# Performance work log

Hardware: AMD Instinct MI355X
Metric: run time of the kernel (lower is better)

The kernel has to match this reference:

```python
import jax, jax.numpy as jnp
import numpy as np

KERNEL_SIZE = 2
DILATION = 2


def aconv(x, A, shift):
    # x: [n, c, v, l], A: [v, w]; temporal roll + zero-mask first `shift` steps,
    # then node diffusion x . A over the node axis.
    xr = jnp.roll(x, shift, axis=3)
    if shift > 0:
        xr = xr.at[..., :shift].set(0.0)
    return jnp.einsum('ncvl,vw->ncwl', xr, A)


def setup_inputs() -> dict:
    key = jax.random.key(0)
    ks = jax.random.split(key, 7)
    N, C, V, L, E, CO = 32, 64, 500, 64, 10, 64
    return {
        'x': jax.random.normal(ks[0], (N, C, V, L), dtype=jnp.float32),
        'nodevec1': jax.random.normal(ks[1], (V, E), dtype=jnp.float32),
        'nodevec2': jax.random.normal(ks[2], (E, V), dtype=jnp.float32),
        'et_w': jax.random.normal(ks[3], (E, E), dtype=jnp.float32),
        'et_b': jax.random.normal(ks[4], (E,), dtype=jnp.float32),
        'mlp_w': jax.random.normal(ks[5], (CO, (1 + KERNEL_SIZE) * C), dtype=jnp.float32) * 0.05,
        'mlp_b': jax.random.normal(ks[6], (CO,), dtype=jnp.float32),
    }


def reference(x, nodevec1, nodevec2, et_w, et_b, mlp_w, mlp_b):
    out = [x]
    x2 = x
    shift = 0
    # hop 0: adaptive adjacency from node embeddings
    adp = jax.nn.softmax(jax.nn.relu(nodevec1 @ nodevec2), axis=1)
    x1 = aconv(x2, adp, shift)
    out.append(x1)
    shift = DILATION
    x2 = x1
    for i in range(KERNEL_SIZE - 1):
        # emb_trans: affine update of both node embeddings
        nodevec1 = nodevec1 @ et_w + et_b
        nodevec2 = (nodevec2.T @ et_w + et_b).T
        adp = jax.nn.softmax(jax.nn.relu(nodevec1 @ nodevec2), axis=1)
        x1 = aconv(x2, adp, shift)
        out.append(x1)
        shift = shift + DILATION
        x2 = x1
    h = jnp.concatenate(out, axis=1)  # [n, (1+K)*c, v, l]
    # 1x1 conv == channel matmul; dropout is identity at inference
    h = jnp.einsum('ncvl,oc->novl', h, mlp_w) + mlp_b[None, :, None, None]
    return h
```

## Files before the change

kernel.cpp:

```cpp
#include <hip/hip_runtime.h>
#include <hip/hip_bf16.h>

#define NB 32
#define CC 64
#define VV 500
#define LL 64
#define EE 10
#define CO 64
#define DIL 2
#define VP 512
#define SL (VV * LL)

typedef unsigned short u16;
typedef unsigned int   u32;
typedef __attribute__((ext_vector_type(8))) short bf16x8;
typedef __attribute__((ext_vector_type(4))) float f32x4;

typedef const __attribute__((address_space(1))) void g_void;
typedef __attribute__((address_space(3))) void l_void;

__device__ __forceinline__ float bf2f(u16 u) {
    union { u32 i; float f; } c; c.i = ((u32)u) << 16; return c.f;
}
__device__ __forceinline__ u16 f2bf(float f) {
    union { float f; u32 i; } c; c.f = f;
    u32 x = c.i;
    u32 r = (x + 0x7fffu + ((x >> 16) & 1u)) >> 16;
    return (u16)r;
}

__global__ void emb_kernel(const float* __restrict__ nv1, const float* __restrict__ nv2,
                           const float* __restrict__ et_w, const float* __restrict__ et_b,
                           const float* __restrict__ mlp_w,
                           float* __restrict__ nv1t, float* __restrict__ nv2t,
                           u16* __restrict__ wb) {
    int idx = blockIdx.x * blockDim.x + threadIdx.x;
    if (idx < VV * EE) {
        int v = idx / EE, e = idx - v * EE;
        float s = et_b[e];
        #pragma unroll
        for (int f = 0; f < EE; f++) s += nv1[v * EE + f] * et_w[f * EE + e];
        nv1t[idx] = s;
    } else if (idx < 2 * VV * EE) {
        int k = idx - VV * EE;
        int e = k / VV, v = k - e * VV;
        float s = et_b[e];
        #pragma unroll
        for (int f = 0; f < EE; f++) s += nv2[f * VV + v] * et_w[f * EE + e];
        nv2t[k] = s;
    } else if (idx < 2 * VV * EE + CO * 3 * CC) {
        int k = idx - 2 * VV * EE;
        wb[k] = f2bf(mlp_w[k]);
    }
}

__global__ __launch_bounds__(64) void adj_kernel(const float* __restrict__ p1,
                                                 const float* __restrict__ p2,
                                                 u16* __restrict__ Atb) {
    const int v = blockIdx.x;
    const int lane = threadIdx.x;
    if (v >= VV) {
        #pragma unroll
        for (int j = 0; j < 8; j++) Atb[(size_t)(lane + 64 * j) * VP + v] = 0;
        return;
    }
    float e1[EE];
    #pragma unroll
    for (int e = 0; e < EE; e++) e1[e] = p1[v * EE + e];

    float r[8];
    float m = -1e30f;
    #pragma unroll
    for (int j = 0; j < 8; j++) {
        int w = lane + 64 * j;
        if (w < VV) {
            float s = 0.f;
            #pragma unroll
            for (int e = 0; e < EE; e++) s += e1[e] * p2[e * VV + w];
            r[j] = fmaxf(s, 0.f);
            m = fmaxf(m, r[j]);
        } else {
            r[j] = -1e30f;
        }
    }
    #pragma unroll
    for (int off = 32; off > 0; off >>= 1) m = fmaxf(m, __shfl_xor(m, off));

    float p[8];
    float sum = 0.f;
    #pragma unroll
    for (int j = 0; j < 8; j++) {
        int w = lane + 64 * j;
        if (w < VV) { p[j] = expf(r[j] - m); sum += p[j]; }
    }
    #pragma unroll
    for (int off = 32; off > 0; off >>= 1) sum += __shfl_xor(sum, off);
    float inv = 1.f / sum;
    #pragma unroll
    for (int j = 0; j < 8; j++) {
        int w = lane + 64 * j;
        Atb[(size_t)w * VP + v] = (w < VV) ? f2bf(p[j] * inv) : (u16)0;
    }
}

__global__ __launch_bounds__(512, 2) void hops_fused(const float* __restrict__ x,
                                                     const u16* __restrict__ Atb0,
                                                     const u16* __restrict__ Atb1,
                                                     u16* __restrict__ x1g,
                                                     u16* __restrict__ x2g) {
    __shared__ u16 Xt[LL * VP];
    __shared__ u16 Ab[2][512 * 32];
    const int nc = blockIdx.x;
    const int tid = threadIdx.x;
    const size_t base = (size_t)nc * (VV * LL);
    const int lane = tid & 63;
    const int wv = tid >> 6;

    int ldsoff[4], rowoff[4];
    #pragma unroll
    for (int j = 0; j < 4; ++j) {
        const int lin = j * 8192 + tid * 16;
        const int w = lin >> 6;
        const int cell = ((lin >> 4) & 3) ^ ((w >> 1) & 3);
        ldsoff[j] = lin;
        rowoff[j] = w * VP + cell * 8;
    }
    char* ab0 = (char*)&Ab[0][0];
    char* ab1 = (char*)&Ab[1][0];

    auto issue_chunk = [&](const u16* Asrc, int kb, char* dst) {
        #pragma unroll
        for (int j = 0; j < 4; ++j)
            __builtin_amdgcn_global_load_lds(
                (g_void*)(Asrc + rowoff[j] + kb),
                (l_void*)(dst + ldsoff[j]), 16, 0, 0);
    };

    issue_chunk(Atb0, 0, ab0);

    {
        char* ldsb = (char*)Xt;
        const int lquad = lane & 15;
        const int vsub = lane >> 4;
        const int l0 = 4 * lquad;
        #pragma unroll
        for (int i = 0; i < 8; ++i) {
            const int vp = wv * 32 + i * 4 + vsub;
            const int v0 = 2 * vp;
            u32 pk0, pk1, pk2, pk3;
            if (v0 < VV) {
                const float* xa = x + base + v0 * LL + l0;
                float4 fa = *(const float4*)xa;
                float4 fb = *(const float4*)(xa + LL);
                pk0 = (u32)f2bf(fa.x) | ((u32)f2bf(fb.x) << 16);
                pk1 = (u32)f2bf(fa.y) | ((u32)f2bf(fb.y) << 16);
                pk2 = (u32)f2bf(fa.z) | ((u32)f2bf(fb.z) << 16);
                pk3 = (u32)f2bf(fa.w) | ((u32)f2bf(fb.w) << 16);
            } else {
                pk0 = pk1 = pk2 = pk3 = 0;
            }
            const int vb = 4 * vp;
            int l = l0;
            *(u32*)(ldsb + l * (VP * 2) + (vb ^ ((l & 7) << 4))) = pk0; l++;
            *(u32*)(ldsb + l * (VP * 2) + (vb ^ ((l & 7) << 4))) = pk1; l++;
            *(u32*)(ldsb + l * (VP * 2) + (vb ^ ((l & 7) << 4))) = pk2; l++;
            *(u32*)(ldsb + l * (VP * 2) + (vb ^ ((l & 7) << 4))) = pk3;
        }
    }
    __syncthreads();

    const int wr = wv * 64;
    const int r15 = lane & 15;
    const int kg = lane >> 4;
    const char* ldsb = (const char*)Xt;
    int lrow[4], lswz[4], aoff[4];
    #pragma unroll
    for (int ct = 0; ct < 4; ct++) {
        const int l = ct * 16 + r15;
        lrow[ct] = l * (VP * 2);
        lswz[ct] = (l & 7) << 4;
    }
    #pragma unroll
    for (int rt = 0; rt < 4; rt++) {
        const int w = wr + rt * 16 + r15;
        aoff[rt] = w * 64 + ((kg ^ ((w >> 1) & 3)) << 4);
    }

    f32x4 acc[4][4];
    #pragma unroll
    for (int rt = 0; rt < 4; rt++)
        #pragma unroll
        for (int ct = 0; ct < 4; ct++)
            acc[rt][ct] = (f32x4){0.f, 0.f, 0.f, 0.f};

    #pragma unroll
    for (int s = 0; s < 16; ++s) {
        const int g1 = s + 1;
        issue_chunk(g1 < 16 ? Atb0 : Atb1, (g1 & 15) * 32, (g1 & 1) ? ab1 : ab0);

        const char* ac = (s & 1) ? ab1 : ab0;
        bf16x8 a[4], b[4];
        #pragma unroll
        for (int rt = 0; rt < 4; rt++)
            a[rt] = *(const bf16x8*)(ac + aoff[rt]);
        #pragma unroll
        for (int ct = 0; ct < 4; ct++)
            b[ct] = *(const bf16x8*)(ldsb + lrow[ct] + ((s * 64 + kg * 16) ^ lswz[ct]));
        #pragma unroll
        for (int rt = 0; rt < 4; rt++)
            #pragma unroll
            for (int ct = 0; ct < 4; ct++)
                acc[rt][ct] = __builtin_amdgcn_mfma_f32_16x16x32_bf16(a[rt], b[ct], acc[rt][ct], 0, 0, 0);
        __syncthreads();
    }

    {
        u16* xo = x1g + base;
        #pragma unroll
        for (int rt = 0; rt < 4; rt++) {
            #pragma unroll
            for (int ct = 0; ct < 4; ct++) {
                const int col = ct * 16 + r15;
                const int wbase = wr + rt * 16 + kg * 4;
                f32x4 c = acc[rt][ct];
                #pragma unroll
                for (int r = 0; r < 4; r++) {
                    int w = wbase + r;
                    if (w < VV) xo[w * LL + col] = f2bf(c[r]);
                }
            }
        }
    }

    {
        char* ldsw = (char*)Xt;
        {
            const int l = tid >> 8;
            const int j = tid & 255;
            *(u32*)(ldsw + l * (VP * 2) + 4 * j) = 0;
        }
        #pragma unroll
        for (int rt = 0; rt < 4; rt++) {
            const int wb2 = (wr + rt * 16 + kg * 4) * 2;
            #pragma unroll
            for (int ct = 0; ct < 4; ct++) {
                const int col = ct * 16 + r15;
                const int ln = col + DIL;
                if (ln < LL) {
                    f32x4 c = acc[rt][ct];
                    u32 plo = (u32)f2bf(c[0]) | ((u32)f2bf(c[1]) << 16);
                    u32 phi = (u32)f2bf(c[2]) | ((u32)f2bf(c[3]) << 16);
                    const int swz = (ln & 7) << 4;
                    char* p = ldsw + ln * (VP * 2);
                    *(u32*)(p + (wb2 ^ swz)) = plo;
                    *(u32*)(p + ((wb2 + 4) ^ swz)) = phi;
                }
            }
        }
    }
    __syncthreads();

    #pragma unroll
    for (int rt = 0; rt < 4; rt++)
        #pragma unroll
        for (int ct = 0; ct < 4; ct++)
            acc[rt][ct] = (f32x4){0.f, 0.f, 0.f, 0.f};

    #pragma unroll
    for (int s = 0; s < 16; ++s) {
        const int g = 16 + s;
        const int g1 = g + 1;
        if (g1 < 32)
            issue_chunk(Atb1, (g1 & 15) * 32, (g1 & 1) ? ab1 : ab0);

        const char* ac = (g & 1) ? ab1 : ab0;
        bf16x8 a[4], b[4];
        #pragma unroll
        for (int rt = 0; rt < 4; rt++)
            a[rt] = *(const bf16x8*)(ac + aoff[rt]);
        #pragma unroll
        for (int ct = 0; ct < 4; ct++)
            b[ct] = *(const bf16x8*)(ldsb + lrow[ct] + ((s * 64 + kg * 16) ^ lswz[ct]));
        #pragma unroll
        for (int rt = 0; rt < 4; rt++)
            #pragma unroll
            for (int ct = 0; ct < 4; ct++)
                acc[rt][ct] = __builtin_amdgcn_mfma_f32_16x16x32_bf16(a[rt], b[ct], acc[rt][ct], 0, 0, 0);
        __syncthreads();
    }

    {
        u16* xo = x2g + base;
        #pragma unroll
        for (int rt = 0; rt < 4; rt++) {
            #pragma unroll
            for (int ct = 0; ct < 4; ct++) {
                const int col = ct * 16 + r15;
                const int wbase = wr + rt * 16 + kg * 4;
                f32x4 c = acc[rt][ct];
                #pragma unroll
                for (int r = 0; r < 4; r++) {
                    int w = wbase + r;
                    if (w < VV) xo[w * LL + col] = f2bf(c[r]);
                }
            }
        }
    }
}

__global__ __launch_bounds__(256, 3) void mlp_mfma(const float* __restrict__ x,
                                                   const u16* __restrict__ x1,
                                                   const u16* __restrict__ x2,
                                                   const u16* __restrict__ wb,
                                                   const float* __restrict__ b,
                                                   float* __restrict__ out) {
    __shared__ u16 Ht[128 * 192];
    const int bid = blockIdx.x;
    const int n = bid / (SL / 128);
    const int st = bid - n * (SL / 128);
    const int s0 = st * 128;
    const int tid = threadIdx.x;

    const int lane = tid & 63;
    const int wv = tid >> 6;
    const int obase = (wv & 1) * 32;
    const int sbase = (wv >> 1) * 64;
    const int r15 = lane & 15;
    const int kg = lane >> 4;

    bf16x8 afrag[2][6];
    #pragma unroll
    for (int rt = 0; rt < 2; rt++)
        #pragma unroll
        for (int ks = 0; ks < 6; ks++)
            afrag[rt][ks] = *(const bf16x8*)(wb + (obase + rt * 16 + r15) * (3 * CC) + ks * 32 + kg * 8);

    {
        char* ldsb = (char*)Ht;
        const int squad = tid >> 3;
        const int pgroup = tid & 7;
        const int sq0 = 4 * squad;
        #pragma unroll
        for (int i = 0; i < 12; ++i) {
            const int P = i * 8 + pgroup;
            const int c = 2 * P;
            u32 pk0, pk1, pk2, pk3;
            if (i < 4) {
                const float* fsrc = x + ((size_t)n * CC + c) * SL + s0 + sq0;
                float4 va = *(const float4*)fsrc;
                float4 vb = *(const float4*)(fsrc + SL);
                pk0 = (u32)f2bf(va.x) | ((u32)f2bf(vb.x) << 16);
                pk1 = (u32)f2bf(va.y) | ((u32)f2bf(vb.y) << 16);
                pk2 = (u32)f2bf(va.z) | ((u32)f2bf(vb.z) << 16);
                pk3 = (u32)f2bf(va.w) | ((u32)f2bf(vb.w) << 16);
            } else {
                const u16* bsrc = (i < 8)
                    ? x1 + ((size_t)n * CC + (c - CC)) * SL + s0 + sq0
                    : x2 + ((size_t)n * CC + (c - 2 * CC)) * SL + s0 + sq0;
                uint2 va = *(const uint2*)bsrc;
                uint2 vb = *(const uint2*)(bsrc + SL);
                pk0 = (va.x & 0xffffu) | (vb.x << 16);
                pk1 = (va.x >> 16) | (vb.x & 0xffff0000u);
                pk2 = (va.y & 0xffffu) | (vb.y << 16);
                pk3 = (va.y >> 16) | (vb.y & 0xffff0000u);
            }
            int s = sq0;
            *(u32*)(ldsb + s * 384 + ((4 * P) ^ ((s & 7) << 4))) = pk0; s++;
            *(u32*)(ldsb + s * 384 + ((4 * P) ^ ((s & 7) << 4))) = pk1; s++;
            *(u32*)(ldsb + s * 384 + ((4 * P) ^ ((s & 7) << 4))) = pk2; s++;
            *(u32*)(ldsb + s * 384 + ((4 * P) ^ ((s & 7) << 4))) = pk3;
        }
    }
    __syncthreads();

    f32x4 acc[2][4];
    #pragma unroll
    for (int rt = 0; rt < 2; rt++)
        #pragma unroll
        for (int ct = 0; ct < 4; ct++)
            acc[rt][ct] = (f32x4){0.f, 0.f, 0.f, 0.f};

    const char* ldsb = (const char*)Ht;
    #pragma unroll
    for (int ks = 0; ks < 6; ks++) {
        bf16x8 bfr[4];
        #pragma unroll
        for (int ct = 0; ct < 4; ct++) {
            const int s = sbase + ct * 16 + r15;
            bfr[ct] = *(const bf16x8*)(ldsb + s * 384 + ((ks * 64 + kg * 16) ^ ((s & 7) << 4)));
        }
        #pragma unroll
        for (int rt = 0; rt < 2; rt++)
            #pragma unroll
            for (int ct = 0; ct < 4; ct++)
                acc[rt][ct] = __builtin_amdgcn_mfma_f32_16x16x32_bf16(afrag[rt][ks], bfr[ct], acc[rt][ct], 0, 0, 0);
    }

    #pragma unroll
    for (int rt = 0; rt < 2; rt++) {
        #pragma unroll
        for (int r = 0; r < 4; r++) {
            const int o = obase + rt * 16 + kg * 4 + r;
            const float bias = b[o];
            float* orow = out + ((size_t)n * CO + o) * SL + s0 + sbase;
            #pragma unroll
            for (int ct = 0; ct < 4; ct++)
                orow[ct * 16 + r15] = acc[rt][ct][r] + bias;
        }
    }
}

extern "C" void kernel_launch(void* const* d_in, const int* in_sizes, int n_in,
                              void* d_out, int out_size, void* d_ws, size_t ws_size,
                              hipStream_t stream) {
    const float* x     = (const float*)d_in[0];
    const float* nv1   = (const float*)d_in[1];
    const float* nv2   = (const float*)d_in[2];
    const float* et_w  = (const float*)d_in[3];
    const float* et_b  = (const float*)d_in[4];
    const float* mlp_w = (const float*)d_in[5];
    const float* mlp_b = (const float*)d_in[6];
    float* out = (float*)d_out;

    char* wsb = (char*)d_ws;
    size_t off = 0;
    auto alloc = [&](size_t bytes) {
        size_t o = off;
        off += (bytes + 255) & ~(size_t)255;
        return o;
    };
    u16*   Atb0 = (u16*)(wsb + alloc((size_t)VP * VP * 2));
    u16*   Atb1 = (u16*)(wsb + alloc((size_t)VP * VP * 2));
    float* nv1t = (float*)(wsb + alloc((size_t)VV * EE * 4));
    float* nv2t = (float*)(wsb + alloc((size_t)EE * VV * 4));
    u16*   wb   = (u16*)(wsb + alloc((size_t)CO * 3 * CC * 2));
    u16*   x1   = (u16*)(wsb + alloc((size_t)NB * CC * VV * LL * 2));
    u16*   x2   = (u16*)(wsb + alloc((size_t)NB * CC * VV * LL * 2));
    (void)in_sizes; (void)n_in; (void)out_size; (void)ws_size;

    const int embN = 2 * VV * EE + CO * 3 * CC;
    emb_kernel<<<(embN + 255) / 256, 256, 0, stream>>>(nv1, nv2, et_w, et_b, mlp_w, nv1t, nv2t, wb);
    adj_kernel<<<VP, 64, 0, stream>>>(nv1, nv2, Atb0);
    adj_kernel<<<VP, 64, 0, stream>>>(nv1t, nv2t, Atb1);
    hops_fused<<<NB * CC, 512, 0, stream>>>(x, Atb0, Atb1, x1, x2);
    mlp_mfma<<<NB * (SL / 128), 256, 0, stream>>>(x, x1, x2, wb, mlp_b, out);
}
```

Baseline: 510.7 us.

## Triple-buffer adjacency chunks with prefetch distance two and explicit waitcnt barriers

```diff
diff --git a/kernel.cpp b/kernel.cpp
--- a/kernel.cpp
+++ b/kernel.cpp
@@ -109,7 +109,7 @@
                                                      u16* __restrict__ x1g,
                                                      u16* __restrict__ x2g) {
     __shared__ u16 Xt[LL * VP];
-    __shared__ u16 Ab[2][512 * 32];
+    __shared__ u16 Ab[3][512 * 32];
     const int nc = blockIdx.x;
     const int tid = threadIdx.x;
     const size_t base = (size_t)nc * (VV * LL);
@@ -125,8 +125,7 @@
         ldsoff[j] = lin;
         rowoff[j] = w * VP + cell * 8;
     }
-    char* ab0 = (char*)&Ab[0][0];
-    char* ab1 = (char*)&Ab[1][0];
+    char* abuf[3] = { (char*)&Ab[0][0], (char*)&Ab[1][0], (char*)&Ab[2][0] };
 
     auto issue_chunk = [&](const u16* Asrc, int kb, char* dst) {
         #pragma unroll
@@ -136,7 +135,8 @@
                 (l_void*)(dst + ldsoff[j]), 16, 0, 0);
     };
 
-    issue_chunk(Atb0, 0, ab0);
+    issue_chunk(Atb0, 0, abuf[0]);
+    issue_chunk(Atb0, 32, abuf[1]);
 
     {
         char* ldsb = (char*)Xt;
@@ -167,7 +167,6 @@
             *(u32*)(ldsb + l * (VP * 2) + (vb ^ ((l & 7) << 4))) = pk3;
         }
     }
-    __syncthreads();
 
     const int wr = wv * 64;
     const int r15 = lane & 15;
@@ -195,10 +194,11 @@
 
     #pragma unroll
     for (int s = 0; s < 16; ++s) {
-        const int g1 = s + 1;
-        issue_chunk(g1 < 16 ? Atb0 : Atb1, (g1 & 15) * 32, (g1 & 1) ? ab1 : ab0);
-
-        const char* ac = (s & 1) ? ab1 : ab0;
+        asm volatile("s_waitcnt vmcnt(4) lgkmcnt(0)\n\ts_barrier" ::: "memory");
+        const int g1 = s + 2;
+        issue_chunk(g1 < 16 ? Atb0 : Atb1, (g1 & 15) * 32, abuf[g1 % 3]);
+
+        const char* ac = abuf[s % 3];
         bf16x8 a[4], b[4];
         #pragma unroll
         for (int rt = 0; rt < 4; rt++)
@@ -211,8 +211,9 @@
             #pragma unroll
             for (int ct = 0; ct < 4; ct++)
                 acc[rt][ct] = __builtin_amdgcn_mfma_f32_16x16x32_bf16(a[rt], b[ct], acc[rt][ct], 0, 0, 0);
-        __syncthreads();
-    }
+    }
+
+    asm volatile("s_waitcnt vmcnt(0) lgkmcnt(0)\n\ts_barrier" ::: "memory");
 
     {
         u16* xo = x1g + base;
@@ -231,7 +232,6 @@
             }
         }
     }
-
     {
         char* ldsw = (char*)Xt;
         {
@@ -258,7 +258,6 @@
             }
         }
     }
-    __syncthreads();
 
     #pragma unroll
     for (int rt = 0; rt < 4; rt++)
@@ -267,26 +266,30 @@
             acc[rt][ct] = (f32x4){0.f, 0.f, 0.f, 0.f};
 
     #pragma unroll
-    for (int s = 0; s < 16; ++s) {
-        const int g = 16 + s;
-        const int g1 = g + 1;
+    for (int s = 16; s < 32; ++s) {
+        if (s <= 17) {
+            asm volatile("s_waitcnt lgkmcnt(0)\n\ts_barrier" ::: "memory");
+        } else {
+            asm volatile("s_waitcnt vmcnt(4) lgkmcnt(0)\n\ts_barrier" ::: "memory");
+        }
+        const int g1 = s + 2;
         if (g1 < 32)
-            issue_chunk(Atb1, (g1 & 15) * 32, (g1 & 1) ? ab1 : ab0);
-
-        const char* ac = (g & 1) ? ab1 : ab0;
+            issue_chunk(Atb1, (g1 & 15) * 32, abuf[g1 % 3]);
+
+        const char* ac = abuf[s % 3];
+        const int kk = s - 16;
         bf16x8 a[4], b[4];
         #pragma unroll
         for (int rt = 0; rt < 4; rt++)
             a[rt] = *(const bf16x8*)(ac + aoff[rt]);
         #pragma unroll
         for (int ct = 0; ct < 4; ct++)
-            b[ct] = *(const bf16x8*)(ldsb + lrow[ct] + ((s * 64 + kg * 16) ^ lswz[ct]));
+            b[ct] = *(const bf16x8*)(ldsb + lrow[ct] + ((kk * 64 + kg * 16) ^ lswz[ct]));
         #pragma unroll
         for (int rt = 0; rt < 4; rt++)
             #pragma unroll
             for (int ct = 0; ct < 4; ct++)
                 acc[rt][ct] = __builtin_amdgcn_mfma_f32_16x16x32_bf16(a[rt], b[ct], acc[rt][ct], 0, 0, 0);
-        __syncthreads();
     }
 
     {
```

After: 462.8 us. 9.4% less time.
